# Optimization experiments

Measured on AMD Instinct MI355X. Metric: run time of the kernel, lower is better.

The kernel has to match this reference:

```python
import jax, jax.numpy as jnp
import numpy as np

F_DIM = 128
EPS = 1e-6
ALPHA_MAX = 0.5


def setup_inputs() -> dict:
    key = jax.random.key(0)
    k1, k2, k3, k4, k5 = jax.random.split(key, 5)
    B, N, C = 64, 16384, 64
    return {
        "x": jax.random.normal(k1, (B, N, C), dtype=jnp.float32),
        "alpha_u": jax.random.uniform(k2, (B, 1, 1, 1), dtype=jnp.float32),
        "select_noise": jax.random.uniform(k3, (B, B), dtype=jnp.float32),
        "domain_labels": jax.random.randint(k4, (B,), 0, 3),
        "class_labels": jax.random.randint(k5, (B,), 0, 4),
    }


def reference(x, alpha_u, select_noise, domain_labels, class_labels):
    B, N, C = x.shape
    t_dim = N // F_DIM
    xr = x.reshape(B, F_DIM, t_dim, C)
    # per-sample, per-channel stats over (freq, time); unbiased var like torch.var
    mu = xr.mean(axis=(1, 2), keepdims=True)                # [B,1,1,C]
    var = jnp.var(xr, axis=(1, 2), ddof=1, keepdims=True)   # [B,1,1,C]
    sig = jnp.sqrt(var + EPS)
    mu = jax.lax.stop_gradient(mu)
    sig = jax.lax.stop_gradient(sig)
    x_normed = (xr - mu) / sig
    # valid mixing partners: same class, different domain
    valid = (class_labels[:, None] == class_labels[None, :]) & \
            (domain_labels[:, None] != domain_labels[None, :])   # [B,B]
    scores = jnp.where(valid, select_noise, -jnp.inf)
    has_valid = valid.any(axis=1)
    idx = jnp.where(has_valid, jnp.argmax(scores, axis=1), jnp.arange(B))
    a = alpha_u * ALPHA_MAX                                  # [B,1,1,1]
    mu2, sig2 = mu[idx], sig[idx]
    mu_mix = mu * a + mu2 * (1.0 - a)
    sig_mix = sig * a + sig2 * (1.0 - a)
    return (x_normed * sig_mix + mu_mix).reshape(B, N, C)
```

## Files before the change

kernel.cpp:

```cpp
#include <hip/hip_runtime.h>
#include <math.h>

#define B_   64
#define N_   16384
#define C_   64
#define S_   16
#define ROWS_PER_BLK (N_ / S_)
#define EPS_ 1e-6f
#define ALPHA_MAX_ 0.5f

typedef float fvec4 __attribute__((ext_vector_type(4)));

__global__ __launch_bounds__(256) void stats_partial_kernel(
    const float* __restrict__ x,
    float* __restrict__ sumP,
    float* __restrict__ sqP)
{
    const int bid = blockIdx.x;
    const int b   = bid >> 4;
    const int s   = bid & 15;

    const float4* xp = (const float4*)(x + ((size_t)b * N_ + (size_t)s * ROWS_PER_BLK) * C_);

    const int tid  = threadIdx.x;
    const int cg   = tid & 15;
    const int row0 = tid >> 4;

    float4 sum = make_float4(0.f, 0.f, 0.f, 0.f);
    float4 sq  = make_float4(0.f, 0.f, 0.f, 0.f);

    for (int r = row0; r < ROWS_PER_BLK; r += 16) {
        float4 v = xp[r * 16 + cg];
        sum.x += v.x; sum.y += v.y; sum.z += v.z; sum.w += v.w;
        sq.x  += v.x * v.x; sq.y += v.y * v.y; sq.z += v.z * v.z; sq.w += v.w * v.w;
    }

    __shared__ float lds[256][8];
    lds[tid][0] = sum.x; lds[tid][1] = sum.y; lds[tid][2] = sum.z; lds[tid][3] = sum.w;
    lds[tid][4] = sq.x;  lds[tid][5] = sq.y;  lds[tid][6] = sq.z;  lds[tid][7] = sq.w;
    __syncthreads();

    for (int off = 128; off >= 16; off >>= 1) {
        if (tid < off) {
            #pragma unroll
            for (int k = 0; k < 8; ++k) lds[tid][k] += lds[tid + off][k];
        }
        __syncthreads();
    }

    if (tid < 16) {
        float* sp = sumP + (size_t)bid * C_ + tid * 4;
        float* qp = sqP  + (size_t)bid * C_ + tid * 4;
        sp[0] = lds[tid][0]; sp[1] = lds[tid][1]; sp[2] = lds[tid][2]; sp[3] = lds[tid][3];
        qp[0] = lds[tid][4]; qp[1] = lds[tid][5]; qp[2] = lds[tid][6]; qp[3] = lds[tid][7];
    }
}

__global__ __launch_bounds__(256) void scale_bias_kernel(
    const float* __restrict__ sumP,
    const float* __restrict__ sqP,
    const float* __restrict__ alpha_u,
    const float* __restrict__ select_noise,
    const int*   __restrict__ dom,
    const int*   __restrict__ cls,
    float* __restrict__ scaleArr,
    float* __restrict__ biasArr)
{
    const int t = blockIdx.x * blockDim.x + threadIdx.x;
    const int b = t >> 6;
    const int c = t & 63;

    const int myCls = cls[b];
    const int myDom = dom[b];
    float best = -1.0f;
    int   bi   = -1;
    for (int j = 0; j < B_; ++j) {
        if (cls[j] == myCls && dom[j] != myDom) {
            float sc = select_noise[b * B_ + j];
            if (sc > best) { best = sc; bi = j; }
        }
    }
    const int idx = (bi < 0) ? b : bi;

    double sum = 0.0, sq = 0.0, sum2 = 0.0, sq2 = 0.0;
    for (int s = 0; s < S_; ++s) {
        sum  += (double)sumP[((size_t)b   * S_ + s) * C_ + c];
        sq   += (double)sqP [((size_t)b   * S_ + s) * C_ + c];
        sum2 += (double)sumP[((size_t)idx * S_ + s) * C_ + c];
        sq2  += (double)sqP [((size_t)idx * S_ + s) * C_ + c];
    }

    const double n = (double)N_;
    const double mu_d   = sum  / n;
    const double var_d  = (sq  - sum  * sum  / n) / (n - 1.0);
    const double mu2_d  = sum2 / n;
    const double var2_d = (sq2 - sum2 * sum2 / n) / (n - 1.0);

    const float mu   = (float)mu_d;
    const float sig  = sqrtf((float)var_d  + EPS_);
    const float mu2  = (float)mu2_d;
    const float sig2 = sqrtf((float)var2_d + EPS_);

    const float a = alpha_u[b] * ALPHA_MAX_;
    const float mu_mix  = mu  * a + mu2  * (1.0f - a);
    const float sig_mix = sig * a + sig2 * (1.0f - a);

    const float scale = sig_mix / sig;
    scaleArr[t] = scale;
    biasArr[t]  = mu_mix - mu * scale;
}

__global__ __launch_bounds__(256) void apply_kernel(
    const float* __restrict__ x,
    const float* __restrict__ scaleArr,
    const float* __restrict__ biasArr,
    float* __restrict__ out)
{
    const int b  = blockIdx.x >> 5;
    const int cg = threadIdx.x & 15;

    const float4 sc = ((const float4*)scaleArr)[b * 16 + cg];
    const float4 bs = ((const float4*)biasArr)[b * 16 + cg];

    const size_t base = (size_t)blockIdx.x * 8192 + threadIdx.x;
    const float4* __restrict__ xin = (const float4*)x;
    fvec4* __restrict__ op = (fvec4*)out;

    #pragma unroll 4
    for (int it = 0; it < 32; ++it) {
        const size_t g = base + (size_t)it * 256;
        float4 v = xin[g];
        fvec4 o;
        o.x = fmaf(v.x, sc.x, bs.x);
        o.y = fmaf(v.y, sc.y, bs.y);
        o.z = fmaf(v.z, sc.z, bs.z);
        o.w = fmaf(v.w, sc.w, bs.w);
        __builtin_nontemporal_store(o, op + g);
    }
}

extern "C" void kernel_launch(void* const* d_in, const int* in_sizes, int n_in,
                              void* d_out, int out_size, void* d_ws, size_t ws_size,
                              hipStream_t stream) {
    const float* x            = (const float*)d_in[0];
    const float* alpha_u      = (const float*)d_in[1];
    const float* select_noise = (const float*)d_in[2];
    const int*   dom          = (const int*)d_in[3];
    const int*   cls          = (const int*)d_in[4];
    float* out = (float*)d_out;

    float* sumP     = (float*)d_ws;
    float* sqP      = sumP + (size_t)B_ * S_ * C_;
    float* scaleArr = sqP  + (size_t)B_ * S_ * C_;
    float* biasArr  = scaleArr + (size_t)B_ * C_;

    stats_partial_kernel<<<B_ * S_, 256, 0, stream>>>(x, sumP, sqP);

    scale_bias_kernel<<<(B_ * C_) / 256, 256, 0, stream>>>(
        sumP, sqP, alpha_u, select_noise, dom, cls, scaleArr, biasArr);

    apply_kernel<<<2048, 256, 0, stream>>>(x, scaleArr, biasArr, out);
}
```

Before: 486.2 us.

## Fuse scale/bias computation into apply kernel and prefetch input during it

Removes the separate scale/bias kernel: each apply block now picks the mixing partner and reduces partial stats for its batch itself, with the per-channel scale and bias kept in shared memory. The first 8 float4 loads per thread are issued before that computation so their latency overlaps it. The stats loop also gets unrolling and FMA accumulation. This saves one launch and a global round trip, but the partner search and fp64 reduction are repeated 32 times per batch and add a block-wide sync.

```diff
diff --git a/kernel.cpp b/kernel.cpp
--- a/kernel.cpp
+++ b/kernel.cpp
@@ -29,10 +29,12 @@
     float4 sum = make_float4(0.f, 0.f, 0.f, 0.f);
     float4 sq  = make_float4(0.f, 0.f, 0.f, 0.f);
 
+    #pragma unroll 8
     for (int r = row0; r < ROWS_PER_BLK; r += 16) {
         float4 v = xp[r * 16 + cg];
         sum.x += v.x; sum.y += v.y; sum.z += v.z; sum.w += v.w;
-        sq.x  += v.x * v.x; sq.y += v.y * v.y; sq.z += v.z * v.z; sq.w += v.w * v.w;
+        sq.x = fmaf(v.x, v.x, sq.x); sq.y = fmaf(v.y, v.y, sq.y);
+        sq.z = fmaf(v.z, v.z, sq.z); sq.w = fmaf(v.w, v.w, sq.w);
     }
 
     __shared__ float lds[256][8];
@@ -56,78 +58,80 @@
     }
 }
 
-__global__ __launch_bounds__(256) void scale_bias_kernel(
+#define PRE 8
+__global__ __launch_bounds__(256) void apply_fused_kernel(
+    const float* __restrict__ x,
     const float* __restrict__ sumP,
     const float* __restrict__ sqP,
     const float* __restrict__ alpha_u,
     const float* __restrict__ select_noise,
     const int*   __restrict__ dom,
     const int*   __restrict__ cls,
-    float* __restrict__ scaleArr,
-    float* __restrict__ biasArr)
-{
-    const int t = blockIdx.x * blockDim.x + threadIdx.x;
-    const int b = t >> 6;
-    const int c = t & 63;
-
-    const int myCls = cls[b];
-    const int myDom = dom[b];
-    float best = -1.0f;
-    int   bi   = -1;
-    for (int j = 0; j < B_; ++j) {
-        if (cls[j] == myCls && dom[j] != myDom) {
-            float sc = select_noise[b * B_ + j];
-            if (sc > best) { best = sc; bi = j; }
-        }
-    }
-    const int idx = (bi < 0) ? b : bi;
-
-    double sum = 0.0, sq = 0.0, sum2 = 0.0, sq2 = 0.0;
-    for (int s = 0; s < S_; ++s) {
-        sum  += (double)sumP[((size_t)b   * S_ + s) * C_ + c];
-        sq   += (double)sqP [((size_t)b   * S_ + s) * C_ + c];
-        sum2 += (double)sumP[((size_t)idx * S_ + s) * C_ + c];
-        sq2  += (double)sqP [((size_t)idx * S_ + s) * C_ + c];
-    }
-
-    const double n = (double)N_;
-    const double mu_d   = sum  / n;
-    const double var_d  = (sq  - sum  * sum  / n) / (n - 1.0);
-    const double mu2_d  = sum2 / n;
-    const double var2_d = (sq2 - sum2 * sum2 / n) / (n - 1.0);
-
-    const float mu   = (float)mu_d;
-    const float sig  = sqrtf((float)var_d  + EPS_);
-    const float mu2  = (float)mu2_d;
-    const float sig2 = sqrtf((float)var2_d + EPS_);
-
-    const float a = alpha_u[b] * ALPHA_MAX_;
-    const float mu_mix  = mu  * a + mu2  * (1.0f - a);
-    const float sig_mix = sig * a + sig2 * (1.0f - a);
-
-    const float scale = sig_mix / sig;
-    scaleArr[t] = scale;
-    biasArr[t]  = mu_mix - mu * scale;
-}
-
-__global__ __launch_bounds__(256) void apply_kernel(
-    const float* __restrict__ x,
-    const float* __restrict__ scaleArr,
-    const float* __restrict__ biasArr,
     float* __restrict__ out)
 {
-    const int b  = blockIdx.x >> 5;
-    const int cg = threadIdx.x & 15;
+    const int tid = threadIdx.x;
+    const int b   = blockIdx.x >> 5;
 
-    const float4 sc = ((const float4*)scaleArr)[b * 16 + cg];
-    const float4 bs = ((const float4*)biasArr)[b * 16 + cg];
-
-    const size_t base = (size_t)blockIdx.x * 8192 + threadIdx.x;
+    const size_t base = (size_t)blockIdx.x * 8192 + tid;
     const float4* __restrict__ xin = (const float4*)x;
     fvec4* __restrict__ op = (fvec4*)out;
 
-    #pragma unroll 4
-    for (int it = 0; it < 32; ++it) {
+    float4 pre[PRE];
+    #pragma unroll
+    for (int it = 0; it < PRE; ++it) pre[it] = xin[base + (size_t)it * 256];
+
+    __shared__ float scb[2][C_];
+    if (tid < C_) {
+        const int myCls = cls[b];
+        const int myDom = dom[b];
+        float best = -1.0f;
+        int   bi   = -1;
+        for (int j = 0; j < B_; ++j) {
+            if (cls[j] == myCls && dom[j] != myDom) {
+                float sc = select_noise[b * B_ + j];
+                if (sc > best) { best = sc; bi = j; }
+            }
+        }
+        const int idx = (bi < 0) ? b : bi;
+
+        double s1 = 0.0, q1 = 0.0, s2 = 0.0, q2 = 0.0;
+        for (int s = 0; s < S_; ++s) {
+            s1 += (double)sumP[((size_t)b   * S_ + s) * C_ + tid];
+            q1 += (double)sqP [((size_t)b   * S_ + s) * C_ + tid];
+            s2 += (double)sumP[((size_t)idx * S_ + s) * C_ + tid];
+            q2 += (double)sqP [((size_t)idx * S_ + s) * C_ + tid];
+        }
+        const double n = (double)N_;
+        const float mu   = (float)(s1 / n);
+        const float sig  = sqrtf((float)((q1 - s1 * s1 / n) / (n - 1.0)) + EPS_);
+        const float mu2  = (float)(s2 / n);
+        const float sig2 = sqrtf((float)((q2 - s2 * s2 / n) / (n - 1.0)) + EPS_);
+
+        const float a = alpha_u[b] * ALPHA_MAX_;
+        const float mu_mix  = mu  * a + mu2  * (1.0f - a);
+        const float sig_mix = sig * a + sig2 * (1.0f - a);
+
+        const float scale = sig_mix / sig;
+        scb[0][tid] = scale;
+        scb[1][tid] = mu_mix - mu * scale;
+    }
+    __syncthreads();
+
+    const int c0 = (tid & 15) * 4;
+    const float4 sc = make_float4(scb[0][c0], scb[0][c0+1], scb[0][c0+2], scb[0][c0+3]);
+    const float4 bs = make_float4(scb[1][c0], scb[1][c0+1], scb[1][c0+2], scb[1][c0+3]);
+
+    #pragma unroll
+    for (int it = 0; it < PRE; ++it) {
+        fvec4 o;
+        o.x = fmaf(pre[it].x, sc.x, bs.x);
+        o.y = fmaf(pre[it].y, sc.y, bs.y);
+        o.z = fmaf(pre[it].z, sc.z, bs.z);
+        o.w = fmaf(pre[it].w, sc.w, bs.w);
+        __builtin_nontemporal_store(o, op + base + (size_t)it * 256);
+    }
+    #pragma unroll 8
+    for (int it = PRE; it < 32; ++it) {
         const size_t g = base + (size_t)it * 256;
         float4 v = xin[g];
         fvec4 o;
@@ -149,15 +153,11 @@
     const int*   cls          = (const int*)d_in[4];
     float* out = (float*)d_out;
 
-    float* sumP     = (float*)d_ws;
-    float* sqP      = sumP + (size_t)B_ * S_ * C_;
-    float* scaleArr = sqP  + (size_t)B_ * S_ * C_;
-    float* biasArr  = scaleArr + (size_t)B_ * C_;
+    float* sumP = (float*)d_ws;
+    float* sqP  = sumP + (size_t)B_ * S_ * C_;
 
     stats_partial_kernel<<<B_ * S_, 256, 0, stream>>>(x, sumP, sqP);
 
-    scale_bias_kernel<<<(B_ * C_) / 256, 256, 0, stream>>>(
-        sumP, sqP, alpha_u, select_noise, dom, cls, scaleArr, biasArr);
-
-    apply_kernel<<<2048, 256, 0, stream>>>(x, scaleArr, biasArr, out);
+    apply_fused_kernel<<<2048, 256, 0, stream>>>(
+        x, sumP, sqP, alpha_u, select_noise, dom, cls, out);
 }
```

Measured after the change: 484.2 us. About the same (-0.4%).
